# Kernel tuning notes

Hardware: AMD Instinct MI355X
Metric: run time of the kernel (lower is better)

## Reference

```python
import jax, jax.numpy as jnp
import numpy as np

B, H, S, D = 2, 16, 2048, 64


def setup_inputs() -> dict:
    key = jax.random.key(0)
    kq, kk, kv = jax.random.split(key, 3)
    Q = jax.random.normal(kq, (B, H, S, D), dtype=jnp.float32)
    K = jax.random.normal(kk, (B, H, S, D), dtype=jnp.float32)
    V = jax.random.normal(kv, (B, H, S, D), dtype=jnp.float32)
    scale = jnp.float32(1.0 / np.sqrt(D))
    # causal mask (1 = keep, 0 = masked), broadcast over batch/heads
    mask = jnp.tril(jnp.ones((S, S), dtype=jnp.int32))[None, None]
    return {"Q": Q, "K": K, "V": V, "scale": scale, "mask": mask}


def reference(Q, K, V, scale, mask):
    # scores: [B,H,S,S] -- intentionally materialized, matching the module
    scores = jnp.einsum("bhqd,bhkd->bhqk", Q, K) * scale
    scores = jnp.where(mask == 0, jnp.float32(-jnp.inf), scores)
    attention_weights = jax.nn.softmax(scores, axis=-1)
    # dropout is identity in eval mode (reference baseline is deterministic)
    output = jnp.einsum("bhqk,bhkd->bhqd", attention_weights, V)
    return output, attention_weights
```

## Files before the change

### kernel.cpp

```cpp
#include <hip/hip_runtime.h>
#include <hip/hip_bf16.h>

#define S_LEN 2048
#define D_DIM 64
#define BH    32
#define BQ    64
#define BK    64
#define NQT   (S_LEN/BQ)
#define KSTR  72
#define NEL   ((size_t)BH * S_LEN * D_DIM)

typedef __attribute__((ext_vector_type(4))) short  short4v;
typedef __attribute__((ext_vector_type(8))) short  short8;
typedef __attribute__((ext_vector_type(4))) float  floatx4;
typedef __attribute__((ext_vector_type(4))) unsigned int uintx4;

__device__ __forceinline__ unsigned short f2bf(float f) {
    unsigned int u = __builtin_bit_cast(unsigned int, f);
    u += 0x7FFFu + ((u >> 16) & 1u);
    return (unsigned short)(u >> 16);
}
__device__ __forceinline__ float bf2f(short s) {
    return __builtin_bit_cast(float, ((unsigned int)(unsigned short)s) << 16);
}

__device__ __forceinline__ short8 load8(const float* p) {
    floatx4 a = *(const floatx4*)p;
    floatx4 b = *(const floatx4*)(p + 4);
    short8 r;
    r[0]=(short)f2bf(a[0]); r[1]=(short)f2bf(a[1]); r[2]=(short)f2bf(a[2]); r[3]=(short)f2bf(a[3]);
    r[4]=(short)f2bf(b[0]); r[5]=(short)f2bf(b[1]); r[6]=(short)f2bf(b[2]); r[7]=(short)f2bf(b[3]);
    return r;
}
__device__ __forceinline__ short8 load8(const __hip_bfloat16* p) {
    return *(const short8*)p;
}
__device__ __forceinline__ void loadrow8(const float* p, unsigned short o[8]) {
    floatx4 a = *(const floatx4*)p, b = *(const floatx4*)(p + 4);
    o[0]=f2bf(a[0]); o[1]=f2bf(a[1]); o[2]=f2bf(a[2]); o[3]=f2bf(a[3]);
    o[4]=f2bf(b[0]); o[5]=f2bf(b[1]); o[6]=f2bf(b[2]); o[7]=f2bf(b[3]);
}
__device__ __forceinline__ void loadrow8(const __hip_bfloat16* p, unsigned short o[8]) {
    short8 v = *(const short8*)p;
#pragma unroll
    for (int j = 0; j < 8; ++j) o[j] = (unsigned short)v[j];
}

template<typename TIN>
__device__ __forceinline__ void prep_body(const TIN* __restrict__ Q, const TIN* __restrict__ K,
                                          const TIN* __restrict__ V,
                                          unsigned short* __restrict__ Qb,
                                          unsigned short* __restrict__ Kb,
                                          unsigned short* __restrict__ Vtg,
                                          unsigned short (*Lt)[KSTR])
{
    const int tid = threadIdx.x;
    const int bid = blockIdx.x;
    {
        size_t idx = ((size_t)bid * 256 + tid) * 16;
        *(short8*)(Qb + idx)     = load8(Q + idx);
        *(short8*)(Qb + idx + 8) = load8(Q + idx + 8);
        *(short8*)(Kb + idx)     = load8(K + idx);
        *(short8*)(Kb + idx + 8) = load8(K + idx + 8);
    }
    const int bh = bid >> 5, st = bid & 31;
    const TIN* Vb = V + ((size_t)bh * S_LEN + (size_t)st * 64) * D_DIM;
#pragma unroll
    for (int i = 0; i < 2; ++i) {
        int flat = tid * 8 + i * 2048;
        int r = flat >> 6, c = flat & 63;
        short8 v = load8(Vb + (size_t)r * D_DIM + c);
        *(short8*)(&Lt[r][c]) = v;
    }
    __syncthreads();
    unsigned short* Vh = Vtg + (size_t)bh * D_DIM * S_LEN;
#pragma unroll
    for (int i = 0; i < 4; ++i) {
        int flat = tid * 4 + i * 1024;
        int d = flat >> 6, sj = flat & 63;
        short4v o;
        o[0] = (short)Lt[sj+0][d]; o[1] = (short)Lt[sj+1][d];
        o[2] = (short)Lt[sj+2][d]; o[3] = (short)Lt[sj+3][d];
        *(short4v*)(Vh + (size_t)d * S_LEN + (size_t)st * 64 + sj) = o;
    }
}

__global__ __launch_bounds__(256)
void prep_kernel(const void* __restrict__ Q, const void* __restrict__ K,
                 const void* __restrict__ V, const void* __restrict__ scp,
                 unsigned short* __restrict__ Qb, unsigned short* __restrict__ Kb,
                 unsigned short* __restrict__ Vtg)
{
    __shared__ unsigned short Lt[64][KSTR];
    const unsigned int sw = *(const unsigned int*)scp;
    if ((sw & 0xFFFFu) == 0u)
        prep_body<float>((const float*)Q, (const float*)K, (const float*)V, Qb, Kb, Vtg, Lt);
    else
        prep_body<__hip_bfloat16>((const __hip_bfloat16*)Q, (const __hip_bfloat16*)K,
                                  (const __hip_bfloat16*)V, Qb, Kb, Vtg, Lt);
}

__device__ __forceinline__ void ldK(const unsigned short* Kh, int kk0, int tid, uintx4 r[2]) {
#pragma unroll
    for (int i = 0; i < 2; ++i)
        r[i] = *(const uintx4*)(Kh + (size_t)kk0 * D_DIM + tid * 8 + i * 2048);
}
__device__ __forceinline__ void ldV(const unsigned short* Vh, int kk0, int tid, uintx4 r[2]) {
#pragma unroll
    for (int i = 0; i < 2; ++i) {
        int flat = tid * 8 + i * 2048;
        r[i] = *(const uintx4*)(Vh + (size_t)(flat >> 6) * S_LEN + kk0 + (flat & 63));
    }
}
__device__ __forceinline__ void st2(unsigned short* dst, int tid, const uintx4 r[2]) {
#pragma unroll
    for (int i = 0; i < 2; ++i) {
        int flat = tid * 8 + i * 2048;
        *(uintx4*)(dst + (flat >> 6) * KSTR + (flat & 63)) = r[i];
    }
}

__global__ __launch_bounds__(256, 4)
void attn_fast(const unsigned short* __restrict__ Qb, const unsigned short* __restrict__ Kb,
               const unsigned short* __restrict__ Vtg, const void* __restrict__ scp,
               float* __restrict__ Out, float* __restrict__ W)
{
    __shared__ unsigned short Kl[2][BK * KSTR];
    __shared__ unsigned short Vt[D_DIM * KSTR];
    __shared__ unsigned short Pl[4][16 * KSTR];

    const int tid  = threadIdx.x;
    const int wave = tid >> 6;
    const int lane = tid & 63;
    const int quad = lane >> 4;
    const int lm   = lane & 15;
    const int idx  = blockIdx.x;
    const int bh   = idx & (BH - 1);
    const int qt   = (NQT - 1) - (idx >> 5);
    const int q0   = qt * BQ;

    const unsigned int sw = *(const unsigned int*)scp;
    const bool isf32 = ((sw & 0xFFFFu) == 0u);
    const float sc = isf32 ? __builtin_bit_cast(float, sw)
                           : __builtin_bit_cast(float, (sw & 0xFFFFu) << 16);
    const float sc2 = sc * 1.44269504088896f;

    float* Ob = Out + (size_t)bh * S_LEN * D_DIM;
    float* Wb = W   + (size_t)bh * S_LEN * S_LEN;
    const unsigned short* Qh = Qb  + (size_t)bh * S_LEN * D_DIM;
    const unsigned short* Kh = Kb  + (size_t)bh * S_LEN * D_DIM;
    const unsigned short* Vh = Vtg + (size_t)bh * D_DIM * S_LEN;

    {
        const int zc = S_LEN - (q0 + BQ);
        floatx4 z4 = {0.f, 0.f, 0.f, 0.f};
        for (int r = 0; r < BQ; ++r) {
            float* wr = Wb + (size_t)(q0 + r) * S_LEN + (q0 + BQ);
            for (int c = tid * 4; c < zc; c += 256 * 4)
                __builtin_nontemporal_store(z4, (floatx4*)(wr + c));
        }
    }

    const int qrow = q0 + wave * 16 + lm;
    const short8 qf0 = *(const short8*)(Qh + (size_t)qrow * D_DIM + quad * 8);
    const short8 qf1 = *(const short8*)(Qh + (size_t)qrow * D_DIM + 32 + quad * 8);

    {
        uintx4 kr[2];
        ldK(Kh, 0, tid, kr); st2(Kl[0], tid, kr);
    }
    __syncthreads();

    float ls0 = 0.f, ls1 = 0.f, ls2 = 0.f, ls3 = 0.f;
    for (int kt = 0; kt <= qt; ++kt) {
        const bool pre = (kt < qt);
        uintx4 kreg[2];
        if (pre) ldK(Kh, (kt + 1) * BK, tid, kreg);
        const unsigned short* Kc = Kl[kt & 1];
        const int kk0 = kt * BK;
        const bool diag = (kt == qt);
#pragma unroll
        for (int kkt = 0; kkt < 4; ++kkt) {
            floatx4 acc = {0.f, 0.f, 0.f, 0.f};
            short8 b0 = *(const short8*)(Kc + (kkt * 16 + lm) * KSTR + quad * 8);
            short8 b1 = *(const short8*)(Kc + (kkt * 16 + lm) * KSTR + 32 + quad * 8);
            acc = __builtin_amdgcn_mfma_f32_16x16x32_bf16(b0, qf0, acc, 0, 0, 0);
            acc = __builtin_amdgcn_mfma_f32_16x16x32_bf16(b1, qf1, acc, 0, 0, 0);
            float s0 = acc[0] * sc2, s1 = acc[1] * sc2;
            float s2 = acc[2] * sc2, s3 = acc[3] * sc2;
            if (diag) {
                int kg = kk0 + kkt * 16 + quad * 4;
                if (kg + 0 > qrow) s0 = -1e30f;
                if (kg + 1 > qrow) s1 = -1e30f;
                if (kg + 2 > qrow) s2 = -1e30f;
                if (kg + 3 > qrow) s3 = -1e30f;
            }
            ls0 += exp2f(s0); ls1 += exp2f(s1);
            ls2 += exp2f(s2); ls3 += exp2f(s3);
        }
        if (pre) st2(Kl[(kt + 1) & 1], tid, kreg);
        __syncthreads();
    }
    float lsum = (ls0 + ls1) + (ls2 + ls3);
    lsum += __shfl_xor(lsum, 16, 64);
    lsum += __shfl_xor(lsum, 32, 64);
    const float linv = 1.0f / lsum;
    float inv_l[4];
    {
        const int srcb = (lane & 48) | ((lane >> 4) << 2);
#pragma unroll
        for (int r = 0; r < 4; ++r) inv_l[r] = __shfl(linv, srcb + r, 64);
    }

    {
        uintx4 kr[2], vr[2];
        ldK(Kh, 0, tid, kr); ldV(Vh, 0, tid, vr);
        st2(Kl[0], tid, kr); st2(Vt, tid, vr);
    }
    __syncthreads();

    floatx4 oacc[4];
#pragma unroll
    for (int dt = 0; dt < 4; ++dt) oacc[dt] = (floatx4){0.f, 0.f, 0.f, 0.f};
    unsigned short* Plw = Pl[wave];

    for (int kt = 0; kt <= qt; ++kt) {
        const bool pre = (kt < qt);
        uintx4 kreg[2], vreg[2];
        if (pre) { ldK(Kh, (kt + 1) * BK, tid, kreg); ldV(Vh, (kt + 1) * BK, tid, vreg); }
        const unsigned short* Kc = Kl[kt & 1];
        const int kk0 = kt * BK;
        const bool diag = (kt == qt);

#pragma unroll
        for (int kkt = 0; kkt < 4; ++kkt) {
            floatx4 acc = {0.f, 0.f, 0.f, 0.f};
            short8 b0 = *(const short8*)(Kc + (kkt * 16 + lm) * KSTR + quad * 8);
            short8 b1 = *(const short8*)(Kc + (kkt * 16 + lm) * KSTR + 32 + quad * 8);
            acc = __builtin_amdgcn_mfma_f32_16x16x32_bf16(qf0, b0, acc, 0, 0, 0);
            acc = __builtin_amdgcn_mfma_f32_16x16x32_bf16(qf1, b1, acc, 0, 0, 0);
#pragma unroll
            for (int r = 0; r < 4; ++r) {
                float s = acc[r] * sc2;
                int rowg = q0 + wave * 16 + quad * 4 + r;
                if (diag && (kk0 + kkt * 16 + lm > rowg)) s = -1e30f;
                float p = exp2f(s) * inv_l[r];
                Plw[(quad * 4 + r) * KSTR + kkt * 16 + lm] = f2bf(p);
            }
        }
        __asm__ volatile("s_waitcnt lgkmcnt(0)" ::: "memory");

        {
            const int rr = lane >> 3, cc = (lane & 7) << 3;
            short8 w0 = *(const short8*)(Plw + rr * KSTR + cc);
            short8 w1 = *(const short8*)(Plw + (8 + rr) * KSTR + cc);
            float* wp0 = Wb + (size_t)(q0 + wave * 16 + rr) * S_LEN + kk0 + cc;
            float* wp1 = wp0 + (size_t)8 * S_LEN;
            floatx4 fa, fb;
#pragma unroll
            for (int j = 0; j < 4; ++j) { fa[j] = bf2f(w0[j]); fb[j] = bf2f(w0[4 + j]); }
            __builtin_nontemporal_store(fa, (floatx4*)wp0);
            __builtin_nontemporal_store(fb, (floatx4*)(wp0 + 4));
#pragma unroll
            for (int j = 0; j < 4; ++j) { fa[j] = bf2f(w1[j]); fb[j] = bf2f(w1[4 + j]); }
            __builtin_nontemporal_store(fa, (floatx4*)wp1);
            __builtin_nontemporal_store(fb, (floatx4*)(wp1 + 4));
        }

#pragma unroll
        for (int c = 0; c < 2; ++c) {
            short8 pf = *(const short8*)(Plw + lm * KSTR + c * 32 + quad * 8);
#pragma unroll
            for (int dt = 0; dt < 4; ++dt) {
                short8 vf = *(const short8*)(Vt + (dt * 16 + lm) * KSTR + c * 32 + quad * 8);
                oacc[dt] = __builtin_amdgcn_mfma_f32_16x16x32_bf16(pf, vf, oacc[dt], 0, 0, 0);
            }
        }

        if (pre) {
            st2(Kl[(kt + 1) & 1], tid, kreg);
            __syncthreads();
            st2(Vt, tid, vreg);
            __syncthreads();
        }
    }

#pragma unroll
    for (int dt = 0; dt < 4; ++dt)
#pragma unroll
        for (int r = 0; r < 4; ++r)
            Ob[(size_t)(q0 + wave * 16 + quad * 4 + r) * D_DIM + dt * 16 + lm] = oacc[dt][r];
}

template<typename TIN>
__device__ __forceinline__ void stageK(const TIN* Kb, int kk0, __hip_bfloat16* Kl, int tid) {
    if constexpr (sizeof(TIN) == 4) {
#pragma unroll
        for (int i = 0; i < 4; ++i) {
            int flat = tid * 4 + i * 1024;
            int row = flat >> 6, col = flat & 63;
            floatx4 v = *(const floatx4*)((const float*)Kb + (size_t)(kk0 + row) * D_DIM + col);
            short4v s;
            s[0]=(short)f2bf(v[0]); s[1]=(short)f2bf(v[1]);
            s[2]=(short)f2bf(v[2]); s[3]=(short)f2bf(v[3]);
            *(short4v*)(&Kl[row * KSTR + col]) = s;
        }
    } else {
#pragma unroll
        for (int i = 0; i < 2; ++i) {
            int flat = tid * 8 + i * 2048;
            int row = flat >> 6, col = flat & 63;
            *(uintx4*)(&Kl[row * KSTR + col]) =
                *(const uintx4*)((const __hip_bfloat16*)Kb + (size_t)(kk0 + row) * D_DIM + col);
        }
    }
}

template<typename TIN>
__device__ __forceinline__ void attn_body(
    const TIN* __restrict__ Qb, const TIN* __restrict__ Kb, const TIN* __restrict__ Vb,
    float sc2, float* __restrict__ Ob, float* __restrict__ Wb,
    int q0, int qt, __hip_bfloat16* Kl, __hip_bfloat16* Vt, __hip_bfloat16* Plw)
{
    const int tid  = threadIdx.x;
    const int wave = tid >> 6;
    const int lane = tid & 63;
    const int quad = lane >> 4;
    const int lm   = lane & 15;

    const int qrow = q0 + wave * 16 + lm;
    short8 qfrag0 = load8(Qb + (size_t)qrow * D_DIM + quad * 8);
    short8 qfrag1 = load8(Qb + (size_t)qrow * D_DIM + 32 + quad * 8);

    float mrow[4], lrow[4];
#pragma unroll
    for (int r = 0; r < 4; ++r) { mrow[r] = -1e30f; lrow[r] = 0.f; }

    for (int kt = 0; kt <= qt; ++kt) {
        const int kk0 = kt * BK;
        __syncthreads();
        stageK(Kb, kk0, Kl, tid);
        __syncthreads();

        const bool diag = (kt == qt);
        float s[4][4];
#pragma unroll
        for (int kkt = 0; kkt < 4; ++kkt) {
            floatx4 acc = {0.f, 0.f, 0.f, 0.f};
            short8 b0 = *(const short8*)(&Kl[(kkt * 16 + lm) * KSTR + quad * 8]);
            short8 b1 = *(const short8*)(&Kl[(kkt * 16 + lm) * KSTR + 32 + quad * 8]);
            acc = __builtin_amdgcn_mfma_f32_16x16x32_bf16(qfrag0, b0, acc, 0, 0, 0);
            acc = __builtin_amdgcn_mfma_f32_16x16x32_bf16(qfrag1, b1, acc, 0, 0, 0);
#pragma unroll
            for (int r = 0; r < 4; ++r) s[kkt][r] = acc[r] * sc2;
            if (diag) {
                int colg = kk0 + kkt * 16 + lm;
#pragma unroll
                for (int r = 0; r < 4; ++r) {
                    int rowg = q0 + wave * 16 + quad * 4 + r;
                    if (colg > rowg) s[kkt][r] = -1e30f;
                }
            }
        }
#pragma unroll
        for (int r = 0; r < 4; ++r) {
            float mx = fmaxf(fmaxf(s[0][r], s[1][r]), fmaxf(s[2][r], s[3][r]));
#pragma unroll
            for (int off = 1; off < 16; off <<= 1)
                mx = fmaxf(mx, __shfl_xor(mx, off, 64));
            float mnew = fmaxf(mrow[r], mx);
            float p = exp2f(s[0][r] - mnew) + exp2f(s[1][r] - mnew) +
                      exp2f(s[2][r] - mnew) + exp2f(s[3][r] - mnew);
#pragma unroll
            for (int off = 1; off < 16; off <<= 1)
                p += __shfl_xor(p, off, 64);
            lrow[r] = lrow[r] * exp2f(mrow[r] - mnew) + p;
            mrow[r] = mnew;
        }
    }

    float inv_l[4];
#pragma unroll
    for (int r = 0; r < 4; ++r) inv_l[r] = 1.0f / lrow[r];

    floatx4 oacc[4];
#pragma unroll
    for (int dt = 0; dt < 4; ++dt) oacc[dt] = (floatx4){0.f, 0.f, 0.f, 0.f};

    for (int kt = 0; kt <= qt; ++kt) {
        const int kk0 = kt * BK;
        __syncthreads();
        stageK(Kb, kk0, Kl, tid);
        {
            int r = tid & 31, c = (tid >> 5) << 3;
            const TIN* v0 = Vb + (size_t)(kk0 + 2 * r) * D_DIM + c;
            unsigned short a[8], b[8];
            loadrow8(v0, a);
            loadrow8(v0 + D_DIM, b);
#pragma unroll
            for (int j = 0; j < 8; ++j) {
                unsigned int d = (unsigned int)a[j] | ((unsigned int)b[j] << 16);
                *(unsigned int*)(&Vt[(c + j) * KSTR + 2 * r]) = d;
            }
        }
        __syncthreads();

        const bool diag = (kt == qt);
        float s[4][4];
#pragma unroll
        for (int kkt = 0; kkt < 4; ++kkt) {
            floatx4 acc = {0.f, 0.f, 0.f, 0.f};
            short8 b0 = *(const short8*)(&Kl[(kkt * 16 + lm) * KSTR + quad * 8]);
            short8 b1 = *(const short8*)(&Kl[(kkt * 16 + lm) * KSTR + 32 + quad * 8]);
            acc = __builtin_amdgcn_mfma_f32_16x16x32_bf16(qfrag0, b0, acc, 0, 0, 0);
            acc = __builtin_amdgcn_mfma_f32_16x16x32_bf16(qfrag1, b1, acc, 0, 0, 0);
#pragma unroll
            for (int r = 0; r < 4; ++r) s[kkt][r] = acc[r] * sc2;
            if (diag) {
                int colg = kk0 + kkt * 16 + lm;
#pragma unroll
                for (int r = 0; r < 4; ++r) {
                    int rowg = q0 + wave * 16 + quad * 4 + r;
                    if (colg > rowg) s[kkt][r] = -1e30f;
                }
            }
        }
#pragma unroll
        for (int kkt = 0; kkt < 4; ++kkt) {
#pragma unroll
            for (int r = 0; r < 4; ++r) {
                float p = exp2f(s[kkt][r] - mrow[r]) * inv_l[r];
                Plw[(quad * 4 + r) * KSTR + kkt * 16 + lm] =
                    __builtin_bit_cast(__hip_bfloat16, f2bf(p));
            }
        }
        __asm__ volatile("s_waitcnt lgkmcnt(0)" ::: "memory");

        {
            int rr = lane >> 3, cc = (lane & 7) << 3;
            short8 w0 = *(const short8*)(&Plw[rr * KSTR + cc]);
            short8 w1 = *(const short8*)(&Plw[(8 + rr) * KSTR + cc]);
            float* wp0 = Wb + (size_t)(q0 + wave * 16 + rr) * S_LEN + kk0 + cc;
            float* wp1 = Wb + (size_t)(q0 + wave * 16 + 8 + rr) * S_LEN + kk0 + cc;
            floatx4 fa, fb;
#pragma unroll
            for (int j = 0; j < 4; ++j) { fa[j] = bf2f(w0[j]); fb[j] = bf2f(w0[4 + j]); }
            *(floatx4*)wp0 = fa; *(floatx4*)(wp0 + 4) = fb;
#pragma unroll
            for (int j = 0; j < 4; ++j) { fa[j] = bf2f(w1[j]); fb[j] = bf2f(w1[4 + j]); }
            *(floatx4*)wp1 = fa; *(floatx4*)(wp1 + 4) = fb;
        }
#pragma unroll
        for (int c = 0; c < 2; ++c) {
            short8 pf = *(const short8*)(&Plw[lm * KSTR + c * 32 + quad * 8]);
#pragma unroll
            for (int dt = 0; dt < 4; ++dt) {
                short8 vf = *(const short8*)(&Vt[(dt * 16 + lm) * KSTR + c * 32 + quad * 8]);
                oacc[dt] = __builtin_amdgcn_mfma_f32_16x16x32_bf16(pf, vf, oacc[dt], 0, 0, 0);
            }
        }
    }

#pragma unroll
    for (int dt = 0; dt < 4; ++dt)
#pragma unroll
        for (int r = 0; r < 4; ++r)
            Ob[(size_t)(q0 + wave * 16 + quad * 4 + r) * D_DIM + dt * 16 + lm] = oacc[dt][r];
}

__global__ __launch_bounds__(256, 4)
void attn_kernel(const void* __restrict__ Q, const void* __restrict__ K,
                 const void* __restrict__ V, const void* __restrict__ scp,
                 float* __restrict__ Out, float* __restrict__ W)
{
    __shared__ __hip_bfloat16 Kl[BK * KSTR];
    __shared__ __hip_bfloat16 Vt[D_DIM * KSTR];
    __shared__ __hip_bfloat16 Pl[4][16 * KSTR];

    const int tid  = threadIdx.x;
    const int wave = tid >> 6;
    const int idx  = blockIdx.x;
    const int bh   = idx & (BH - 1);
    const int qt   = (NQT - 1) - (idx >> 5);
    const int q0   = qt * BQ;

    const size_t bqd = (size_t)bh * S_LEN * D_DIM;
    float* Ob = Out + bqd;
    float* Wb = W + (size_t)bh * S_LEN * S_LEN;

    const unsigned int sw = *(const unsigned int*)scp;
    const bool isf32 = ((sw & 0xFFFFu) == 0u);
    const float sc = isf32 ? __builtin_bit_cast(float, sw)
                           : __builtin_bit_cast(float, (sw & 0xFFFFu) << 16);
    const float sc2 = sc * 1.44269504088896f;

    {
        const int zc = S_LEN - (q0 + BQ);
        floatx4 z4 = {0.f, 0.f, 0.f, 0.f};
        for (int r = 0; r < BQ; ++r) {
            float* wr = Wb + (size_t)(q0 + r) * S_LEN + (q0 + BQ);
            for (int c = tid * 4; c < zc; c += 256 * 4)
                *(floatx4*)(wr + c) = z4;
        }
    }

    if (isf32)
        attn_body<float>((const float*)Q + bqd, (const float*)K + bqd,
                         (const float*)V + bqd, sc2, Ob, Wb, q0, qt, Kl, Vt, Pl[wave]);
    else
        attn_body<__hip_bfloat16>((const __hip_bfloat16*)Q + bqd, (const __hip_bfloat16*)K + bqd,
                                  (const __hip_bfloat16*)V + bqd, sc2, Ob, Wb, q0, qt, Kl, Vt, Pl[wave]);
}

extern "C" void kernel_launch(void* const* d_in, const int* in_sizes, int n_in,
                              void* d_out, int out_size, void* d_ws, size_t ws_size,
                              hipStream_t stream) {
    float* Outp = (float*)d_out;
    float* Wp   = Outp + NEL;

    const size_t need = NEL * 3 * sizeof(unsigned short);
    if (d_ws != nullptr && ws_size >= need) {
        unsigned short* Qb  = (unsigned short*)d_ws;
        unsigned short* Kb  = Qb + NEL;
        unsigned short* Vtg = Kb + NEL;
        prep_kernel<<<dim3(NQT * BH), dim3(256), 0, stream>>>(
            d_in[0], d_in[1], d_in[2], d_in[3], Qb, Kb, Vtg);
        attn_fast<<<dim3(NQT * BH), dim3(256), 0, stream>>>(
            Qb, Kb, Vtg, d_in[3], Outp, Wp);
    } else {
        attn_kernel<<<dim3(NQT * BH), dim3(256), 0, stream>>>(
            d_in[0], d_in[1], d_in[2], d_in[3], Outp, Wp);
    }
}
```

Baseline: 735.4 us.

## Keep P in registers via transposed MFMA and lane swaps, double-buffer V

The second pass now computes S transposed (K as the A operand), so each lane holds four consecutive key columns of one query row. It writes the fp32 attention weights straight to global with one 16-byte nontemporal store and packs P to bf16 with v_cvt_pk_bf16_f32. The P fragment for the PV MFMA is then built with permlane32/permlane16 swaps instead of a round trip through the LDS P buffer. V is double-buffered so one barrier per tile replaces two. This removes LDS traffic, the LDS wait and a sync, in exchange for inline asm and a larger V footprint in LDS.

```diff
diff --git a/kernel.cpp b/kernel.cpp
--- a/kernel.cpp
+++ b/kernel.cpp
@@ -126,8 +126,7 @@
                float* __restrict__ Out, float* __restrict__ W)
 {
     __shared__ unsigned short Kl[2][BK * KSTR];
-    __shared__ unsigned short Vt[D_DIM * KSTR];
-    __shared__ unsigned short Pl[4][16 * KSTR];
+    __shared__ unsigned short Vl[2][D_DIM * KSTR];
 
     const int tid  = threadIdx.x;
     const int wave = tid >> 6;
@@ -205,82 +204,74 @@
     lsum += __shfl_xor(lsum, 16, 64);
     lsum += __shfl_xor(lsum, 32, 64);
     const float linv = 1.0f / lsum;
-    float inv_l[4];
-    {
-        const int srcb = (lane & 48) | ((lane >> 4) << 2);
-#pragma unroll
-        for (int r = 0; r < 4; ++r) inv_l[r] = __shfl(linv, srcb + r, 64);
-    }
 
     {
         uintx4 kr[2], vr[2];
         ldK(Kh, 0, tid, kr); ldV(Vh, 0, tid, vr);
-        st2(Kl[0], tid, kr); st2(Vt, tid, vr);
+        st2(Kl[0], tid, kr); st2(Vl[0], tid, vr);
     }
     __syncthreads();
 
     floatx4 oacc[4];
 #pragma unroll
     for (int dt = 0; dt < 4; ++dt) oacc[dt] = (floatx4){0.f, 0.f, 0.f, 0.f};
-    unsigned short* Plw = Pl[wave];
 
     for (int kt = 0; kt <= qt; ++kt) {
         const bool pre = (kt < qt);
         uintx4 kreg[2], vreg[2];
         if (pre) { ldK(Kh, (kt + 1) * BK, tid, kreg); ldV(Vh, (kt + 1) * BK, tid, vreg); }
         const unsigned short* Kc = Kl[kt & 1];
+        const unsigned short* Vc = Vl[kt & 1];
         const int kk0 = kt * BK;
         const bool diag = (kt == qt);
 
+        unsigned int dd[4][2];
 #pragma unroll
         for (int kkt = 0; kkt < 4; ++kkt) {
             floatx4 acc = {0.f, 0.f, 0.f, 0.f};
             short8 b0 = *(const short8*)(Kc + (kkt * 16 + lm) * KSTR + quad * 8);
             short8 b1 = *(const short8*)(Kc + (kkt * 16 + lm) * KSTR + 32 + quad * 8);
-            acc = __builtin_amdgcn_mfma_f32_16x16x32_bf16(qf0, b0, acc, 0, 0, 0);
-            acc = __builtin_amdgcn_mfma_f32_16x16x32_bf16(qf1, b1, acc, 0, 0, 0);
-#pragma unroll
-            for (int r = 0; r < 4; ++r) {
-                float s = acc[r] * sc2;
-                int rowg = q0 + wave * 16 + quad * 4 + r;
-                if (diag && (kk0 + kkt * 16 + lm > rowg)) s = -1e30f;
-                float p = exp2f(s) * inv_l[r];
-                Plw[(quad * 4 + r) * KSTR + kkt * 16 + lm] = f2bf(p);
-            }
-        }
-        __asm__ volatile("s_waitcnt lgkmcnt(0)" ::: "memory");
-
-        {
-            const int rr = lane >> 3, cc = (lane & 7) << 3;
-            short8 w0 = *(const short8*)(Plw + rr * KSTR + cc);
-            short8 w1 = *(const short8*)(Plw + (8 + rr) * KSTR + cc);
-            float* wp0 = Wb + (size_t)(q0 + wave * 16 + rr) * S_LEN + kk0 + cc;
-            float* wp1 = wp0 + (size_t)8 * S_LEN;
-            floatx4 fa, fb;
-#pragma unroll
-            for (int j = 0; j < 4; ++j) { fa[j] = bf2f(w0[j]); fb[j] = bf2f(w0[4 + j]); }
-            __builtin_nontemporal_store(fa, (floatx4*)wp0);
-            __builtin_nontemporal_store(fb, (floatx4*)(wp0 + 4));
-#pragma unroll
-            for (int j = 0; j < 4; ++j) { fa[j] = bf2f(w1[j]); fb[j] = bf2f(w1[4 + j]); }
-            __builtin_nontemporal_store(fa, (floatx4*)wp1);
-            __builtin_nontemporal_store(fb, (floatx4*)(wp1 + 4));
-        }
-
+            acc = __builtin_amdgcn_mfma_f32_16x16x32_bf16(b0, qf0, acc, 0, 0, 0);
+            acc = __builtin_amdgcn_mfma_f32_16x16x32_bf16(b1, qf1, acc, 0, 0, 0);
+            const int kg = kk0 + kkt * 16 + quad * 4;
+            float s0 = acc[0] * sc2, s1 = acc[1] * sc2;
+            float s2 = acc[2] * sc2, s3 = acc[3] * sc2;
+            if (diag) {
+                if (kg + 0 > qrow) s0 = -1e30f;
+                if (kg + 1 > qrow) s1 = -1e30f;
+                if (kg + 2 > qrow) s2 = -1e30f;
+                if (kg + 3 > qrow) s3 = -1e30f;
+            }
+            float p0 = exp2f(s0) * linv, p1 = exp2f(s1) * linv;
+            float p2 = exp2f(s2) * linv, p3 = exp2f(s3) * linv;
+            floatx4 w4; w4[0] = p0; w4[1] = p1; w4[2] = p2; w4[3] = p3;
+            __builtin_nontemporal_store(w4, (floatx4*)(Wb + (size_t)qrow * S_LEN + kg));
+            asm("v_cvt_pk_bf16_f32 %0, %1, %2" : "=v"(dd[kkt][0]) : "v"(p0), "v"(p1));
+            asm("v_cvt_pk_bf16_f32 %0, %1, %2" : "=v"(dd[kkt][1]) : "v"(p2), "v"(p3));
+        }
 #pragma unroll
         for (int c = 0; c < 2; ++c) {
-            short8 pf = *(const short8*)(Plw + lm * KSTR + c * 32 + quad * 8);
+            asm("v_permlane32_swap_b32 %0, %1" : "+v"(dd[2*c][0]), "+v"(dd[2*c+1][0]));
+            asm("v_permlane32_swap_b32 %0, %1" : "+v"(dd[2*c][1]), "+v"(dd[2*c+1][1]));
+            asm("v_permlane16_swap_b32 %0, %1" : "+v"(dd[2*c][0]), "+v"(dd[2*c+1][0]));
+            asm("v_permlane16_swap_b32 %0, %1" : "+v"(dd[2*c][1]), "+v"(dd[2*c+1][1]));
+        }
+#pragma unroll
+        for (int c = 0; c < 2; ++c) {
+            uintx4 pv_;
+            pv_[0] = dd[2*c][0]; pv_[1] = dd[2*c][1];
+            pv_[2] = dd[2*c+1][0]; pv_[3] = dd[2*c+1][1];
+            short8 pf = __builtin_bit_cast(short8, pv_);
 #pragma unroll
             for (int dt = 0; dt < 4; ++dt) {
-                short8 vf = *(const short8*)(Vt + (dt * 16 + lm) * KSTR + c * 32 + quad * 8);
+                short8 vf = *(const short8*)(Vc + (dt * 16 + lm) * KSTR + c * 32 + quad * 8);
                 oacc[dt] = __builtin_amdgcn_mfma_f32_16x16x32_bf16(pf, vf, oacc[dt], 0, 0, 0);
             }
         }
 
         if (pre) {
             st2(Kl[(kt + 1) & 1], tid, kreg);
-            __syncthreads();
-            st2(Vt, tid, vreg);
+            st2(Vl[(kt + 1) & 1], tid, vreg);
             __syncthreads();
         }
     }
```

Measured after the change: 679.2 us. 7.7% less time.
